# Optimization experiments

Measured on AMD Instinct MI355X. Metric: run time of the kernel, lower is better.

Reference implementation:

```python
import jax, jax.numpy as jnp
import numpy as np

N, E, C, ED = 50000, 800000, 128, 16
NEG_SLOPE = 0.2


def setup_inputs() -> dict:
    key = jax.random.key(0)
    ks = jax.random.split(key, 18)
    inp = {
        "h": jax.random.normal(ks[0], (N, C), jnp.float32),
        "edge_index": jax.random.randint(ks[1], (2, E), 0, N),
        "edge_attr": jax.random.normal(ks[2], (E, ED), jnp.float32),
        "reducible": jax.random.randint(ks[3], (N,), 0, 2) > 0,
    }
    names = ["W", "att_src", "att_dst", "W_edge", "att_edge", "W_res", "bias"]
    shapes = [(C, C), (C,), (C,), (ED, C), (C,), (C, C), (C,)]
    i = 4
    for pre in ["red_", "irr_"]:
        for n, sh in zip(names, shapes):
            inp[pre + n] = jax.random.normal(ks[i], sh, jnp.float32) * 0.05
            i += 1
    return inp


def _gat_conv(h, src, dst, edge_attr, W, att_src, att_dst, W_edge, att_edge, W_res, bias):
    """PyG GATConv (heads=1, residual=True, add_self_loops=True, fill_value='mean')."""
    n = h.shape[0]
    # self-loop edge_attr = mean of incoming edge_attr per node (0 if none)
    sum_attr = jax.ops.segment_sum(edge_attr, dst, num_segments=n)
    cnt = jax.ops.segment_sum(jnp.ones((edge_attr.shape[0],), edge_attr.dtype), dst, num_segments=n)
    mean_attr = sum_attr / jnp.maximum(cnt, 1.0)[:, None]
    loop = jnp.arange(n)
    s = jnp.concatenate([src, loop])   # [E+N]
    d = jnp.concatenate([dst, loop])   # [E+N]
    ea = jnp.concatenate([edge_attr, mean_attr], axis=0)  # [E+N, ED]
    x = h @ W                              # [N, C]
    a_src = x @ att_src                    # [N]
    a_dst = x @ att_dst                    # [N]
    a_edge = (ea @ W_edge) @ att_edge      # [E+N]
    alpha = jax.nn.leaky_relu(a_src[s] + a_dst[d] + a_edge, NEG_SLOPE)
    # per-destination softmax (every node has a self-loop -> denom > 0)
    m = jax.ops.segment_max(alpha, d, num_segments=n)
    ex = jnp.exp(alpha - m[d])
    denom = jax.ops.segment_sum(ex, d, num_segments=n)
    w = ex / denom[d]                      # [E+N]
    out = jax.ops.segment_sum(w[:, None] * x[s], d, num_segments=n)  # [N, C]
    return out + h @ W_res + bias


def reference(h, edge_index, edge_attr, reducible,
              red_W, red_att_src, red_att_dst, red_W_edge, red_att_edge, red_W_res, red_bias,
              irr_W, irr_att_src, irr_att_dst, irr_W_edge, irr_att_edge, irr_W_res, irr_bias):
    src, dst = edge_index[0], edge_index[1]
    out_r = _gat_conv(h, src, dst, edge_attr, red_W, red_att_src, red_att_dst,
                      red_W_edge, red_att_edge, red_W_res, red_bias)
    out_i = _gat_conv(h, src, dst, edge_attr, irr_W, irr_att_src, irr_att_dst,
                      irr_W_edge, irr_att_edge, irr_W_res, irr_bias)
    return jax.nn.relu(jnp.where(reducible[:, None], out_r, out_i))
```

## Files before the change

kernel.cpp:

```cpp
#include <hip/hip_runtime.h>
#include <hip/hip_bf16.h>

#define CDIM 128
#define EDIM 16
#define NEG_SLOPE 0.2f

typedef __attribute__((ext_vector_type(8))) short bf16x8;
typedef __attribute__((ext_vector_type(4))) float f32x4;
typedef unsigned int uint;
typedef unsigned short ushort;

__device__ __forceinline__ ushort f2bf(float f) {
    uint u = __float_as_uint(f);
    return (ushort)((u + 0x7fffu + ((u >> 16) & 1u)) >> 16);
}
__device__ __forceinline__ uint packbf(float lo, float hi) {
    return ((uint)f2bf(hi) << 16) | (uint)f2bf(lo);
}
__device__ __forceinline__ float bflo(uint w) { return __uint_as_float(w << 16); }
__device__ __forceinline__ float bfhi(uint w) { return __uint_as_float(w & 0xffff0000u); }

__device__ __forceinline__ bool redtest(const void* red, int i, int notInt, int notFloat) {
    if (!notInt)        return ((const int*)red)[i] != 0;
    else if (!notFloat) return ((const float*)red)[i] != 0.f;
    else                return ((const unsigned char*)red)[i] != 0;
}

__global__ void bcatwe_kernel(const float* __restrict__ Wr, const float* __restrict__ Wi,
                              const float* __restrict__ Wrr, const float* __restrict__ Wri,
                              ushort* __restrict__ BT,
                              const float* __restrict__ WeR, const float* __restrict__ aeR,
                              const float* __restrict__ WeI, const float* __restrict__ aeI,
                              float* __restrict__ we) {
    if (blockIdx.x < 256) {
        int idx = blockIdx.x * 256 + threadIdx.x;
        int c = idx >> 7, k = idx & 127;
        const float* srcm;
        if (c < 128)      srcm = Wr;
        else if (c < 256) srcm = Wi;
        else if (c < 384) srcm = Wrr;
        else              srcm = Wri;
        BT[idx] = f2bf(srcm[k * 128 + (c & 127)]);
    } else {
        int lane = threadIdx.x;
        if (lane < 16) {
            float s = 0.f;
            for (int c = 0; c < CDIM; ++c) s += WeR[lane * CDIM + c] * aeR[c];
            we[lane] = s;
        } else if (lane < 32) {
            int j = lane - 16;
            float s = 0.f;
            for (int c = 0; c < CDIM; ++c) s += WeI[j * CDIM + c] * aeI[c];
            we[16 + j] = s;
        }
    }
}

__global__ __launch_bounds__(256) void prep_kernel(const uint* __restrict__ red, int nwords,
                                                   int* __restrict__ flags,
                                                   const int* __restrict__ dst, int* __restrict__ cnt,
                                                   int* __restrict__ rank,
                                                   const float* __restrict__ ea, const float* __restrict__ we,
                                                   uint* __restrict__ escal4,
                                                   const float* __restrict__ h, ushort* __restrict__ hbf,
                                                   int E, int n4) {
    int i = blockIdx.x * 256 + threadIdx.x;
    if (i < nwords) {
        uint w = red[i];
        bool isInt = (w <= 1u);
        bool isFloat = (w == 0u) || (w == 0x3f800000u);
        if (!isInt) atomicOr(&flags[0], 1);
        if (!isFloat) atomicOr(&flags[1], 1);
    }
    if (i < E) {
        rank[i] = atomicAdd(&cnt[dst[i]], 1);
        const float4* row = (const float4*)(ea + (size_t)i * EDIM);
        const float4* we4 = (const float4*)we;
        float er = 0.f, ei = 0.f;
#pragma unroll
        for (int q = 0; q < 4; ++q) {
            float4 v = row[q];
            float4 wr = we4[q], wi = we4[4 + q];
            er += v.x * wr.x + v.y * wr.y + v.z * wr.z + v.w * wr.w;
            ei += v.x * wi.x + v.y * wi.y + v.z * wi.z + v.w * wi.w;
        }
        escal4[i] = packbf(er, ei);
    }
    if (i < n4) {
        float4 v = ((const float4*)h)[i];
        ushort4 o;
        o.x = f2bf(v.x); o.y = f2bf(v.y); o.z = f2bf(v.z); o.w = f2bf(v.w);
        ((ushort4*)hbf)[i] = o;
    }
}

__global__ __launch_bounds__(256) void gemm_dots(const ushort* __restrict__ A,
                                                 const ushort* __restrict__ BT,
                                                 ushort* __restrict__ C,
                                                 const float* __restrict__ attsr, const float* __restrict__ attdr,
                                                 const float* __restrict__ attsi, const float* __restrict__ attdi,
                                                 float* __restrict__ asr, float* __restrict__ adr,
                                                 float* __restrict__ asi, float* __restrict__ adi, int M) {
    __shared__ ushort As[128 * 128];
    __shared__ ushort Bs[128 * 128];
    __shared__ float dots[2][128];
    int t = threadIdx.x;
    int lane = t & 63, wv = t >> 6;
    int rb = blockIdx.x * 128, cb = blockIdx.y * 128;
    int by = blockIdx.y;

    if (t < 128) { dots[0][t] = 0.f; dots[1][t] = 0.f; }

    int rsub = wv * 4 + (lane >> 4);
    int c0 = lane & 15;
#pragma unroll
    for (int p = 0; p < 8; ++p) {
        int row = p * 16 + rsub;
        int chunk = c0 ^ (row & 7);
        int gra = rb + row; if (gra > M - 1) gra = M - 1;
        const ushort* ga = A + (size_t)gra * 128 + chunk * 8;
        __builtin_amdgcn_global_load_lds(
            (const __attribute__((address_space(1))) void*)ga,
            (__attribute__((address_space(3))) void*)((char*)As + p * 4096 + wv * 1024),
            16, 0, 0);
        const ushort* gb = BT + (size_t)(cb + row) * 128 + chunk * 8;
        __builtin_amdgcn_global_load_lds(
            (const __attribute__((address_space(1))) void*)gb,
            (__attribute__((address_space(3))) void*)((char*)Bs + p * 4096 + wv * 1024),
            16, 0, 0);
    }
    __syncthreads();

    int wr = wv >> 1, wc = wv & 1;
    int l15 = lane & 15, l4 = lane >> 4;
    f32x4 acc[4][4];
#pragma unroll
    for (int i = 0; i < 4; ++i)
#pragma unroll
        for (int j = 0; j < 4; ++j) acc[i][j] = (f32x4){0.f, 0.f, 0.f, 0.f};

    const char* Ab = (const char*)As;
    const char* Bb = (const char*)Bs;
#pragma unroll
    for (int ks = 0; ks < 4; ++ks) {
        bf16x8 a[4], b[4];
#pragma unroll
        for (int f = 0; f < 4; ++f) {
            int row = wr * 64 + f * 16 + l15;
            int ch = (ks * 4 + l4) ^ (row & 7);
            a[f] = *(const bf16x8*)(Ab + row * 256 + ch * 16);
            int col = wc * 64 + f * 16 + l15;
            int ch2 = (ks * 4 + l4) ^ (col & 7);
            b[f] = *(const bf16x8*)(Bb + col * 256 + ch2 * 16);
        }
#pragma unroll
        for (int i = 0; i < 4; ++i)
#pragma unroll
            for (int j = 0; j < 4; ++j)
                acc[i][j] = __builtin_amdgcn_mfma_f32_16x16x32_bf16(a[i], b[j], acc[i][j], 0, 0, 0);
    }

    if (by < 2) {
        const float* attS = by ? attsi : attsr;
        const float* attD = by ? attdi : attdr;
        float aS[4], aD[4];
#pragma unroll
        for (int j = 0; j < 4; ++j) {
            int c = wc * 64 + j * 16 + l15;
            aS[j] = attS[c]; aD[j] = attD[c];
        }
#pragma unroll
        for (int i = 0; i < 4; ++i)
#pragma unroll
            for (int rr = 0; rr < 4; ++rr) {
                float ps = 0.f, pd = 0.f;
#pragma unroll
                for (int j = 0; j < 4; ++j) {
                    float v = acc[i][j][rr];
                    ps += v * aS[j]; pd += v * aD[j];
                }
#pragma unroll
                for (int d = 1; d < 16; d <<= 1) {
                    ps += __shfl_xor(ps, d); pd += __shfl_xor(pd, d);
                }
                if (l15 == 0) {
                    int row = wr * 64 + i * 16 + l4 * 4 + rr;
                    atomicAdd(&dots[0][row], ps);
                    atomicAdd(&dots[1][row], pd);
                }
            }
    }

#pragma unroll
    for (int i = 0; i < 4; ++i) {
        int rl = wr * 64 + i * 16 + l4 * 4;
#pragma unroll
        for (int j = 0; j < 4; ++j) {
            int col = cb + wc * 64 + j * 16 + l15;
#pragma unroll
            for (int r = 0; r < 4; ++r) {
                int gr = rb + rl + r;
                if (gr < M) C[(size_t)gr * 512 + col] = f2bf(acc[i][j][r]);
            }
        }
    }

    if (by < 2) {
        __syncthreads();
        if (t < 128) {
            int gr = rb + t;
            if (gr < M) {
                if (by == 0) { asr[gr] = dots[0][t]; adr[gr] = dots[1][t]; }
                else         { asi[gr] = dots[0][t]; adi[gr] = dots[1][t]; }
            }
        }
    }
}

__global__ __launch_bounds__(256) void scanA_kernel(const int* __restrict__ cnt,
                                                    int* __restrict__ offv,
                                                    int* __restrict__ bsum, int n) {
    __shared__ int wsum[4];
    int t = threadIdx.x, lane = t & 63, wid = t >> 6;
    int i0 = blockIdx.x * 1024 + t * 4;
    int v[4];
#pragma unroll
    for (int j = 0; j < 4; ++j) { int i = i0 + j; v[j] = (i < n) ? cnt[i] : 0; }
    int s = v[0] + v[1] + v[2] + v[3];
    int incl = s;
#pragma unroll
    for (int d = 1; d < 64; d <<= 1) { int u = __shfl_up(incl, d); if (lane >= d) incl += u; }
    if (lane == 63) wsum[wid] = incl;
    __syncthreads();
    int wpre = 0;
    for (int w = 0; w < wid; ++w) wpre += wsum[w];
    int run = wpre + incl - s;
#pragma unroll
    for (int j = 0; j < 4; ++j) {
        int i = i0 + j;
        if (i < n) offv[i] = run;
        run += v[j];
    }
    if (t == 255) bsum[blockIdx.x] = wpre + incl;
}

__global__ void scanB_kernel(int* __restrict__ bsum, int* __restrict__ offv, int nb, int n) {
    int lane = threadIdx.x;
    int carry = 0;
    for (int base = 0; base < nb; base += 64) {
        int i = base + lane;
        int v = (i < nb) ? bsum[i] : 0;
        int incl = v;
#pragma unroll
        for (int d = 1; d < 64; d <<= 1) { int u = __shfl_up(incl, d); if (lane >= d) incl += u; }
        if (i < nb) bsum[i] = carry + incl - v;
        carry += __shfl(incl, 63);
    }
    if (lane == 0) offv[n] = carry;
}

__global__ __launch_bounds__(256) void scanC_kernel(int* __restrict__ offv,
                                                    const int* __restrict__ bsum, int n) {
    int add = bsum[blockIdx.x];
    int i0 = blockIdx.x * 1024 + threadIdx.x * 4;
#pragma unroll
    for (int j = 0; j < 4; ++j) {
        int i = i0 + j;
        if (i < n) offv[i] += add;
    }
}

__global__ __launch_bounds__(256) void scatter_kernel(
    const int* __restrict__ src, const int* __restrict__ dst,
    const int* __restrict__ rank, const uint* __restrict__ escal4,
    const void* __restrict__ red, const int* __restrict__ flags,
    const int* __restrict__ offv, uint* __restrict__ csr, int E) {
    int e = blockIdx.x * 256 + threadIdx.x;
    if (e >= E) return;
    int s = src[e], d = dst[e];
    uint ee = escal4[e];
    int notInt = flags[0], notFloat = flags[1];
    bool rr = redtest(red, d, notInt, notFloat);
    uint evb = rr ? (ee & 0xffffu) : (ee >> 16);
    csr[offv[d] + rank[e]] = (uint)s | (evb << 16);
}

__global__ __launch_bounds__(256) void node_kernel(
    const ushort* __restrict__ xcat,
    const float* __restrict__ adst_r, const float* __restrict__ adst_i,
    const float* __restrict__ asrc_r, const float* __restrict__ asrc_i,
    const void* __restrict__ red, const int* __restrict__ flags,
    const int* __restrict__ offv, const uint* __restrict__ csr,
    const float* __restrict__ bias_r, const float* __restrict__ bias_i,
    float* __restrict__ out, int n) {
    __shared__ uint2 buf[4][64];
    int wv = threadIdx.x >> 6, lane = threadIdx.x & 63;
    int node = blockIdx.x * 4 + wv;
    if (node >= n) return;

    int notInt = flags[0], notFloat = flags[1];
    bool r = redtest(red, node, notInt, notFloat);

    const float* asrc = r ? asrc_r : asrc_i;
    float adst = (r ? adst_r : adst_i)[node];
    uint vsel = r ? 0u : 256u;
    int b0 = offv[node], b1 = offv[node + 1];
    int k = b1 - b0;
    const char* xb = (const char*)xcat;
    uint lane4 = lane * 4;

    float m = -1e30f, denom = 0.f;
    float acc0a = 0.f, acc1a = 0.f, acc0b = 0.f, acc1b = 0.f;
    float sumE = 0.f;

    for (int base = b0; base < b1; base += 64) {
        int j = base + lane;
        float al = -1e30f; uint soff = 0;
        if (j < b1) {
            uint rec = csr[j];
            uint s = rec & 0xffffu;
            float ev = bfhi(rec);
            sumE += ev;
            soff = s * 1024u + vsel;
            float a = asrc[s] + ev + adst;
            al = (a >= 0.f) ? a : NEG_SLOPE * a;
        }
        float cm = al;
#pragma unroll
        for (int d = 32; d; d >>= 1) cm = fmaxf(cm, __shfl_xor(cm, d));
        float mn = fmaxf(m, cm);
        float sc = __expf(m - mn);
        denom *= sc; acc0a *= sc; acc1a *= sc; acc0b *= sc; acc1b *= sc;
        m = mn;
        float ex = (j < b1) ? __expf(al - mn) : 0.f;
        buf[wv][lane] = make_uint2(__float_as_uint(ex), soff);
        __builtin_amdgcn_wave_barrier();
        int cc = min(64, b1 - base);
        int ccp = (cc + 7) & ~7;
        for (int tq = 0; tq < ccp; tq += 8) {
            uint2 u[8];
#pragma unroll
            for (int q = 0; q < 8; ++q) u[q] = buf[wv][tq + q];
            uint v[8];
#pragma unroll
            for (int q = 0; q < 8; ++q) v[q] = *(const uint*)(xb + u[q].y + lane4);
#pragma unroll
            for (int q = 0; q < 4; ++q) {
                float w = __uint_as_float(u[q].x);
                acc0a += w * bflo(v[q]); acc1a += w * bfhi(v[q]);
            }
#pragma unroll
            for (int q = 4; q < 8; ++q) {
                float w = __uint_as_float(u[q].x);
                acc0b += w * bflo(v[q]); acc1b += w * bfhi(v[q]);
            }
        }
        float exs = ex;
#pragma unroll
        for (int d = 32; d; d >>= 1) exs += __shfl_xor(exs, d);
        denom += exs;
        __builtin_amdgcn_wave_barrier();
    }
    float acc0 = acc0a + acc0b, acc1 = acc1a + acc1b;

#pragma unroll
    for (int d = 32; d; d >>= 1) sumE += __shfl_xor(sumE, d);
    float eself = sumE / fmaxf((float)k, 1.f);
    float a = asrc[node] + adst + eself;
    float aself = (a >= 0.f) ? a : NEG_SLOPE * a;
    float mn = fmaxf(m, aself);
    float sc = __expf(m - mn);
    float exl = __expf(aself - mn);
    denom = denom * sc + exl;
    uint voff = (uint)node * 1024u + vsel;
    uint vsw = *(const uint*)(xb + voff + lane4);
    acc0 = acc0 * sc + exl * bflo(vsw);
    acc1 = acc1 * sc + exl * bfhi(vsw);

    float inv = 1.f / denom;
    uint roff = (uint)node * 1024u + (r ? 512u : 768u);
    uint bw = *(const uint*)(xb + roff + lane4);
    float2 bi2 = ((const float2*)(r ? bias_r : bias_i))[lane];
    float o0 = acc0 * inv + bflo(bw) + bi2.x;
    float o1 = acc1 * inv + bfhi(bw) + bi2.y;
    ((float2*)out)[(size_t)node * 64 + lane] = make_float2(fmaxf(o0, 0.f), fmaxf(o1, 0.f));
}

extern "C" void kernel_launch(void* const* d_in, const int* in_sizes, int n_in,
                              void* d_out, int out_size, void* d_ws, size_t ws_size,
                              hipStream_t stream) {
    const float* h          = (const float*)d_in[0];
    const int*   edge_index = (const int*)d_in[1];
    const float* edge_attr  = (const float*)d_in[2];
    const void*  reducible  = d_in[3];
    const float* red_W      = (const float*)d_in[4];
    const float* red_att_src= (const float*)d_in[5];
    const float* red_att_dst= (const float*)d_in[6];
    const float* red_W_edge = (const float*)d_in[7];
    const float* red_att_edge=(const float*)d_in[8];
    const float* red_W_res  = (const float*)d_in[9];
    const float* red_bias   = (const float*)d_in[10];
    const float* irr_W      = (const float*)d_in[11];
    const float* irr_att_src= (const float*)d_in[12];
    const float* irr_att_dst= (const float*)d_in[13];
    const float* irr_W_edge = (const float*)d_in[14];
    const float* irr_att_edge=(const float*)d_in[15];
    const float* irr_W_res  = (const float*)d_in[16];
    const float* irr_bias   = (const float*)d_in[17];

    const int N = in_sizes[0] / CDIM;
    const int E = in_sizes[1] / 2;
    const int* src = edge_index;
    const int* dst = edge_index + E;
    const int nb = (N + 1023) / 1024;
    const int n4 = N * 128 / 4;

    float* out = (float*)d_out;

    size_t cur = 0;
    auto alloc = [&](size_t bytes) { size_t p = cur; cur = (cur + bytes + 255) & ~(size_t)255; return p; };
    char* ws = (char*)d_ws;
    size_t o_xcat  = alloc((size_t)N * 512 * 2);
    size_t o_hbf   = alloc((size_t)N * 128 * 2);
    size_t o_bcat  = alloc(512 * 128 * 2);
    size_t o_we    = alloc(256);
    size_t o_asr   = alloc((size_t)N * 4);
    size_t o_adr   = alloc((size_t)N * 4);
    size_t o_asi   = alloc((size_t)N * 4);
    size_t o_adi   = alloc((size_t)N * 4);
    size_t o_flags = alloc(256);
    size_t o_cnt   = alloc((size_t)N * 4);
    size_t o_off   = alloc((size_t)(N + 1) * 4);
    size_t o_bsum  = alloc((size_t)(nb + 1) * 4);
    size_t o_rank  = alloc((size_t)E * 4);
    size_t o_escal = alloc((size_t)E * 4);
    size_t o_csr   = alloc((size_t)E * 4);
    if (cur > ws_size) return;

    ushort* xcat = (ushort*)(ws + o_xcat);
    ushort* hbf  = (ushort*)(ws + o_hbf);
    ushort* bcat = (ushort*)(ws + o_bcat);
    float* we    = (float*)(ws + o_we);
    float* asr   = (float*)(ws + o_asr);
    float* adr   = (float*)(ws + o_adr);
    float* asi   = (float*)(ws + o_asi);
    float* adi   = (float*)(ws + o_adi);
    int*   flags = (int*)(ws + o_flags);
    int*   cnt   = (int*)(ws + o_cnt);
    int*   offv  = (int*)(ws + o_off);
    int*   bsum  = (int*)(ws + o_bsum);
    int*   rank  = (int*)(ws + o_rank);
    uint*  escal4= (uint*)(ws + o_escal);
    uint*  csr   = (uint*)(ws + o_csr);

    hipMemsetAsync(flags, 0, 8, stream);
    hipMemsetAsync(cnt, 0, (size_t)N * 4, stream);

    bcatwe_kernel<<<257, 256, 0, stream>>>(red_W, irr_W, red_W_res, irr_W_res, bcat,
                                           red_W_edge, red_att_edge, irr_W_edge, irr_att_edge, we);

    int nwords = N / 4;
    int pgrid = (max(E, n4) + 255) / 256;
    prep_kernel<<<pgrid, 256, 0, stream>>>((const uint*)reducible, nwords, flags,
                                           dst, cnt, rank, edge_attr, we, escal4,
                                           h, hbf, E, n4);

    dim3 ggrid((N + 127) / 128, 4);
    gemm_dots<<<ggrid, 256, 0, stream>>>(hbf, bcat, xcat,
                                         red_att_src, red_att_dst,
                                         irr_att_src, irr_att_dst,
                                         asr, adr, asi, adi, N);

    scanA_kernel<<<nb, 256, 0, stream>>>(cnt, offv, bsum, N);
    scanB_kernel<<<1, 64, 0, stream>>>(bsum, offv, nb, N);
    scanC_kernel<<<nb, 256, 0, stream>>>(offv, bsum, N);

    scatter_kernel<<<(E + 255) / 256, 256, 0, stream>>>(src, dst, rank, escal4,
                                                        reducible, flags, offv, csr, E);

    node_kernel<<<(N + 3) / 4, 256, 0, stream>>>(xcat, adr, adi, asr, asi,
                                                 reducible, flags, offv, csr,
                                                 red_bias, irr_bias, out, N);
}
```

Before: 148.8 us.

## Fuse bf16 conversion of h into GEMM, drop scanC, add nontemporal accesses

Removes the separate h-to-bf16 pass from the prep kernel and has the GEMM load fp32 h directly, converting and swizzling it into LDS itself. It also drops the scanC kernel by having the scatter and node kernels add block sums to the local offsets on the fly. It marks streaming loads and stores as nontemporal as well. Together these cut one launch and an N×128 bf16 round trip through memory. The cost is that the GEMM's A-tile load goes through registers instead of an async global-to-LDS copy, and each offset lookup needs an extra read.

```diff
diff --git a/kernel.cpp b/kernel.cpp
--- a/kernel.cpp
+++ b/kernel.cpp
@@ -7,6 +7,7 @@
 
 typedef __attribute__((ext_vector_type(8))) short bf16x8;
 typedef __attribute__((ext_vector_type(4))) float f32x4;
+typedef __attribute__((ext_vector_type(2))) float f32x2;
 typedef unsigned int uint;
 typedef unsigned short ushort;
 
@@ -61,9 +62,7 @@
                                                    const int* __restrict__ dst, int* __restrict__ cnt,
                                                    int* __restrict__ rank,
                                                    const float* __restrict__ ea, const float* __restrict__ we,
-                                                   uint* __restrict__ escal4,
-                                                   const float* __restrict__ h, ushort* __restrict__ hbf,
-                                                   int E, int n4) {
+                                                   uint* __restrict__ escal4, int E) {
     int i = blockIdx.x * 256 + threadIdx.x;
     if (i < nwords) {
         uint w = red[i];
@@ -73,28 +72,23 @@
         if (!isFloat) atomicOr(&flags[1], 1);
     }
     if (i < E) {
-        rank[i] = atomicAdd(&cnt[dst[i]], 1);
-        const float4* row = (const float4*)(ea + (size_t)i * EDIM);
+        int r = atomicAdd(&cnt[dst[i]], 1);
+        __builtin_nontemporal_store(r, rank + i);
+        const f32x4* row = (const f32x4*)(ea + (size_t)i * EDIM);
         const float4* we4 = (const float4*)we;
         float er = 0.f, ei = 0.f;
 #pragma unroll
         for (int q = 0; q < 4; ++q) {
-            float4 v = row[q];
+            f32x4 v = __builtin_nontemporal_load(row + q);
             float4 wr = we4[q], wi = we4[4 + q];
             er += v.x * wr.x + v.y * wr.y + v.z * wr.z + v.w * wr.w;
             ei += v.x * wi.x + v.y * wi.y + v.z * wi.z + v.w * wi.w;
         }
-        escal4[i] = packbf(er, ei);
-    }
-    if (i < n4) {
-        float4 v = ((const float4*)h)[i];
-        ushort4 o;
-        o.x = f2bf(v.x); o.y = f2bf(v.y); o.z = f2bf(v.z); o.w = f2bf(v.w);
-        ((ushort4*)hbf)[i] = o;
-    }
-}
-
-__global__ __launch_bounds__(256) void gemm_dots(const ushort* __restrict__ A,
+        __builtin_nontemporal_store(packbf(er, ei), escal4 + i);
+    }
+}
+
+__global__ __launch_bounds__(256) void gemm_dots(const float* __restrict__ h,
                                                  const ushort* __restrict__ BT,
                                                  ushort* __restrict__ C,
                                                  const float* __restrict__ attsr, const float* __restrict__ attdr,
@@ -117,17 +111,26 @@
     for (int p = 0; p < 8; ++p) {
         int row = p * 16 + rsub;
         int chunk = c0 ^ (row & 7);
-        int gra = rb + row; if (gra > M - 1) gra = M - 1;
-        const ushort* ga = A + (size_t)gra * 128 + chunk * 8;
-        __builtin_amdgcn_global_load_lds(
-            (const __attribute__((address_space(1))) void*)ga,
-            (__attribute__((address_space(3))) void*)((char*)As + p * 4096 + wv * 1024),
-            16, 0, 0);
         const ushort* gb = BT + (size_t)(cb + row) * 128 + chunk * 8;
         __builtin_amdgcn_global_load_lds(
             (const __attribute__((address_space(1))) void*)gb,
             (__attribute__((address_space(3))) void*)((char*)Bs + p * 4096 + wv * 1024),
             16, 0, 0);
+    }
+
+    {
+        int row = t >> 1, half = t & 1;
+        int gra = rb + row; if (gra > M - 1) gra = M - 1;
+        const float4* hp = (const float4*)(h + (size_t)gra * 128 + half * 64);
+#pragma unroll
+        for (int k = 0; k < 8; ++k) {
+            float4 a = hp[2 * k], b = hp[2 * k + 1];
+            uint4 o;
+            o.x = packbf(a.x, a.y); o.y = packbf(a.z, a.w);
+            o.z = packbf(b.x, b.y); o.w = packbf(b.z, b.w);
+            int c = half * 8 + k;
+            *(uint4*)((char*)As + row * 256 + (c ^ (row & 7)) * 16) = o;
+        }
     }
     __syncthreads();
 
@@ -218,7 +221,7 @@
 }
 
 __global__ __launch_bounds__(256) void scanA_kernel(const int* __restrict__ cnt,
-                                                    int* __restrict__ offv,
+                                                    int* __restrict__ offA,
                                                     int* __restrict__ bsum, int n) {
     __shared__ int wsum[4];
     int t = threadIdx.x, lane = t & 63, wid = t >> 6;
@@ -238,13 +241,13 @@
 #pragma unroll
     for (int j = 0; j < 4; ++j) {
         int i = i0 + j;
-        if (i < n) offv[i] = run;
+        if (i < n) offA[i] = run;
         run += v[j];
     }
     if (t == 255) bsum[blockIdx.x] = wpre + incl;
 }
 
-__global__ void scanB_kernel(int* __restrict__ bsum, int* __restrict__ offv, int nb, int n) {
+__global__ void scanB_kernel(int* __restrict__ bsum, int nb) {
     int lane = threadIdx.x;
     int carry = 0;
     for (int base = 0; base < nb; base += 64) {
@@ -256,33 +259,25 @@
         if (i < nb) bsum[i] = carry + incl - v;
         carry += __shfl(incl, 63);
     }
-    if (lane == 0) offv[n] = carry;
-}
-
-__global__ __launch_bounds__(256) void scanC_kernel(int* __restrict__ offv,
-                                                    const int* __restrict__ bsum, int n) {
-    int add = bsum[blockIdx.x];
-    int i0 = blockIdx.x * 1024 + threadIdx.x * 4;
-#pragma unroll
-    for (int j = 0; j < 4; ++j) {
-        int i = i0 + j;
-        if (i < n) offv[i] += add;
-    }
 }
 
 __global__ __launch_bounds__(256) void scatter_kernel(
     const int* __restrict__ src, const int* __restrict__ dst,
     const int* __restrict__ rank, const uint* __restrict__ escal4,
     const void* __restrict__ red, const int* __restrict__ flags,
-    const int* __restrict__ offv, uint* __restrict__ csr, int E) {
+    const int* __restrict__ offA, const int* __restrict__ bsum,
+    uint* __restrict__ csr, int E) {
     int e = blockIdx.x * 256 + threadIdx.x;
     if (e >= E) return;
-    int s = src[e], d = dst[e];
-    uint ee = escal4[e];
+    int s = __builtin_nontemporal_load(src + e);
+    int d = __builtin_nontemporal_load(dst + e);
+    uint ee = __builtin_nontemporal_load(escal4 + e);
+    int rk = __builtin_nontemporal_load(rank + e);
     int notInt = flags[0], notFloat = flags[1];
     bool rr = redtest(red, d, notInt, notFloat);
     uint evb = rr ? (ee & 0xffffu) : (ee >> 16);
-    csr[offv[d] + rank[e]] = (uint)s | (evb << 16);
+    int off = offA[d] + bsum[d >> 10];
+    csr[off + rk] = (uint)s | (evb << 16);
 }
 
 __global__ __launch_bounds__(256) void node_kernel(
@@ -290,9 +285,10 @@
     const float* __restrict__ adst_r, const float* __restrict__ adst_i,
     const float* __restrict__ asrc_r, const float* __restrict__ asrc_i,
     const void* __restrict__ red, const int* __restrict__ flags,
-    const int* __restrict__ offv, const uint* __restrict__ csr,
+    const int* __restrict__ offA, const int* __restrict__ bsum,
+    const uint* __restrict__ csr,
     const float* __restrict__ bias_r, const float* __restrict__ bias_i,
-    float* __restrict__ out, int n) {
+    float* __restrict__ out, int n, int E) {
     __shared__ uint2 buf[4][64];
     int wv = threadIdx.x >> 6, lane = threadIdx.x & 63;
     int node = blockIdx.x * 4 + wv;
@@ -304,20 +300,21 @@
     const float* asrc = r ? asrc_r : asrc_i;
     float adst = (r ? adst_r : adst_i)[node];
     uint vsel = r ? 0u : 256u;
-    int b0 = offv[node], b1 = offv[node + 1];
+    int b0 = offA[node] + bsum[node >> 10];
+    int b1 = (node + 1 < n) ? (offA[node + 1] + bsum[(node + 1) >> 10]) : E;
     int k = b1 - b0;
     const char* xb = (const char*)xcat;
     uint lane4 = lane * 4;
 
     float m = -1e30f, denom = 0.f;
-    float acc0a = 0.f, acc1a = 0.f, acc0b = 0.f, acc1b = 0.f;
+    float2 acca = make_float2(0.f, 0.f), accb = make_float2(0.f, 0.f);
     float sumE = 0.f;
 
     for (int base = b0; base < b1; base += 64) {
         int j = base + lane;
         float al = -1e30f; uint soff = 0;
         if (j < b1) {
-            uint rec = csr[j];
+            uint rec = __builtin_nontemporal_load(csr + j);
             uint s = rec & 0xffffu;
             float ev = bfhi(rec);
             sumE += ev;
@@ -330,7 +327,8 @@
         for (int d = 32; d; d >>= 1) cm = fmaxf(cm, __shfl_xor(cm, d));
         float mn = fmaxf(m, cm);
         float sc = __expf(m - mn);
-        denom *= sc; acc0a *= sc; acc1a *= sc; acc0b *= sc; acc1b *= sc;
+        denom *= sc;
+        acca.x *= sc; acca.y *= sc; accb.x *= sc; accb.y *= sc;
         m = mn;
         float ex = (j < b1) ? __expf(al - mn) : 0.f;
         buf[wv][lane] = make_uint2(__float_as_uint(ex), soff);
@@ -347,12 +345,12 @@
 #pragma unroll
             for (int q = 0; q < 4; ++q) {
                 float w = __uint_as_float(u[q].x);
-                acc0a += w * bflo(v[q]); acc1a += w * bfhi(v[q]);
+                acca.x += w * bflo(v[q]); acca.y += w * bfhi(v[q]);
             }
 #pragma unroll
             for (int q = 4; q < 8; ++q) {
                 float w = __uint_as_float(u[q].x);
-                acc0b += w * bflo(v[q]); acc1b += w * bfhi(v[q]);
+                accb.x += w * bflo(v[q]); accb.y += w * bfhi(v[q]);
             }
         }
         float exs = ex;
@@ -361,7 +359,7 @@
         denom += exs;
         __builtin_amdgcn_wave_barrier();
     }
-    float acc0 = acc0a + acc0b, acc1 = acc1a + acc1b;
+    float acc0 = acca.x + accb.x, acc1 = acca.y + accb.y;
 
 #pragma unroll
     for (int d = 32; d; d >>= 1) sumE += __shfl_xor(sumE, d);
@@ -381,9 +379,10 @@
     uint roff = (uint)node * 1024u + (r ? 512u : 768u);
     uint bw = *(const uint*)(xb + roff + lane4);
     float2 bi2 = ((const float2*)(r ? bias_r : bias_i))[lane];
-    float o0 = acc0 * inv + bflo(bw) + bi2.x;
-    float o1 = acc1 * inv + bfhi(bw) + bi2.y;
-    ((float2*)out)[(size_t)node * 64 + lane] = make_float2(fmaxf(o0, 0.f), fmaxf(o1, 0.f));
+    f32x2 o;
+    o.x = fmaxf(acc0 * inv + bflo(bw) + bi2.x, 0.f);
+    o.y = fmaxf(acc1 * inv + bfhi(bw) + bi2.y, 0.f);
+    __builtin_nontemporal_store(o, ((f32x2*)out) + (size_t)node * 64 + lane);
 }
 
 extern "C" void kernel_launch(void* const* d_in, const int* in_sizes, int n_in,
@@ -413,7 +412,6 @@
     const int* src = edge_index;
     const int* dst = edge_index + E;
     const int nb = (N + 1023) / 1024;
-    const int n4 = N * 128 / 4;
 
     float* out = (float*)d_out;
 
@@ -421,7 +419,6 @@
     auto alloc = [&](size_t bytes) { size_t p = cur; cur = (cur + bytes + 255) & ~(size_t)255; return p; };
     char* ws = (char*)d_ws;
     size_t o_xcat  = alloc((size_t)N * 512 * 2);
-    size_t o_hbf   = alloc((size_t)N * 128 * 2);
     size_t o_bcat  = alloc(512 * 128 * 2);
     size_t o_we    = alloc(256);
     size_t o_asr   = alloc((size_t)N * 4);
@@ -430,7 +427,7 @@
     size_t o_adi   = alloc((size_t)N * 4);
     size_t o_flags = alloc(256);
     size_t o_cnt   = alloc((size_t)N * 4);
-    size_t o_off   = alloc((size_t)(N + 1) * 4);
+    size_t o_offA  = alloc((size_t)N * 4);
     size_t o_bsum  = alloc((size_t)(nb + 1) * 4);
     size_t o_rank  = alloc((size_t)E * 4);
     size_t o_escal = alloc((size_t)E * 4);
@@ -438,7 +435,6 @@
     if (cur > ws_size) return;
 
     ushort* xcat = (ushort*)(ws + o_xcat);
-    ushort* hbf  = (ushort*)(ws + o_hbf);
     ushort* bcat = (ushort*)(ws + o_bcat);
     float* we    = (float*)(ws + o_we);
     float* asr   = (float*)(ws + o_asr);
@@ -447,7 +443,7 @@
     float* adi   = (float*)(ws + o_adi);
     int*   flags = (int*)(ws + o_flags);
     int*   cnt   = (int*)(ws + o_cnt);
-    int*   offv  = (int*)(ws + o_off);
+    int*   offA  = (int*)(ws + o_offA);
     int*   bsum  = (int*)(ws + o_bsum);
     int*   rank  = (int*)(ws + o_rank);
     uint*  escal4= (uint*)(ws + o_escal);
@@ -460,25 +456,22 @@
                                            red_W_edge, red_att_edge, irr_W_edge, irr_att_edge, we);
 
     int nwords = N / 4;
-    int pgrid = (max(E, n4) + 255) / 256;
-    prep_kernel<<<pgrid, 256, 0, stream>>>((const uint*)reducible, nwords, flags,
-                                           dst, cnt, rank, edge_attr, we, escal4,
-                                           h, hbf, E, n4);
+    prep_kernel<<<(E + 255) / 256, 256, 0, stream>>>((const uint*)reducible, nwords, flags,
+                                                     dst, cnt, rank, edge_attr, we, escal4, E);
 
     dim3 ggrid((N + 127) / 128, 4);
-    gemm_dots<<<ggrid, 256, 0, stream>>>(hbf, bcat, xcat,
+    gemm_dots<<<ggrid, 256, 0, stream>>>(h, bcat, xcat,
                                          red_att_src, red_att_dst,
                                          irr_att_src, irr_att_dst,
                                          asr, adr, asi, adi, N);
 
-    scanA_kernel<<<nb, 256, 0, stream>>>(cnt, offv, bsum, N);
-    scanB_kernel<<<1, 64, 0, stream>>>(bsum, offv, nb, N);
-    scanC_kernel<<<nb, 256, 0, stream>>>(offv, bsum, N);
+    scanA_kernel<<<nb, 256, 0, stream>>>(cnt, offA, bsum, N);
+    scanB_kernel<<<1, 64, 0, stream>>>(bsum, nb);
 
     scatter_kernel<<<(E + 255) / 256, 256, 0, stream>>>(src, dst, rank, escal4,
-                                                        reducible, flags, offv, csr, E);
+                                                        reducible, flags, offA, bsum, csr, E);
 
     node_kernel<<<(N + 3) / 4, 256, 0, stream>>>(xcat, adr, adi, asr, asi,
-                                                 reducible, flags, offv, csr,
-                                                 red_bias, irr_bias, out, N);
-}
+                                                 reducible, flags, offA, bsum, csr,
+                                                 red_bias, irr_bias, out, N, E);
+}
```

After: 169.2 us (median of 4 runs). 1.14x slower.
